# Kernel optimization log

Measured on AMD Instinct MI355X. Metric: run time of the kernel, lower is better.

Reference implementation:

```python
import jax, jax.numpy as jnp
import numpy as np

B = 4; T = 4; C = 1; H = 128; W = 128; P = 16; D = 384; DEPTH = 4
DIN = 768; N = 16; DTR = 24; K = 4
GH = (T * H) // P; GW = W // P; NTOK = GH * GW; POS = NTOK // 2  # middle cls token
SDIM = 16; ADIM = 4


def setup_inputs() -> dict:
    ks = iter(jax.random.split(jax.random.key(0), 48))
    def rn(shape, s=0.02):
        return jax.random.normal(next(ks), shape, jnp.float32) * s
    inp = {}
    inp["depth_seq"] = jax.random.normal(next(ks), (B, T, C, H, W), jnp.float32)
    inp["state_vec"] = jax.random.normal(next(ks), (B, SDIM), jnp.float32)
    inp["action"] = jax.random.normal(next(ks), (B, ADIM), jnp.float32)
    inp["patch_w"] = rn((D, C * P * P)); inp["patch_b"] = jnp.zeros((D,), jnp.float32)
    inp["cls_token"] = rn((1, 1, D)); inp["pos_embed"] = rn((1, NTOK + 1, D))
    inp["ln_w"] = jnp.ones((DEPTH, D), jnp.float32); inp["ln_b"] = jnp.zeros((DEPTH, D), jnp.float32)
    inp["in_proj_w"] = rn((DEPTH, 2 * DIN, D))
    inp["conv_w"] = rn((DEPTH, DIN, K), 0.2); inp["conv_b"] = jnp.zeros((DEPTH, DIN), jnp.float32)
    inp["conv_wb"] = rn((DEPTH, DIN, K), 0.2); inp["conv_bb"] = jnp.zeros((DEPTH, DIN), jnp.float32)
    inp["xproj_w"] = rn((DEPTH, DTR + 2 * N, DIN)); inp["xproj_wb"] = rn((DEPTH, DTR + 2 * N, DIN))
    inp["dtproj_w"] = rn((DEPTH, DIN, DTR), 0.1); inp["dtproj_b"] = jnp.full((DEPTH, DIN), -4.0, jnp.float32)
    inp["dtproj_wb"] = rn((DEPTH, DIN, DTR), 0.1); inp["dtproj_bb"] = jnp.full((DEPTH, DIN), -4.0, jnp.float32)
    Ainit = jnp.log(jnp.tile(jnp.arange(1, N + 1, dtype=jnp.float32)[None, None, :], (DEPTH, DIN, 1)))
    inp["A_log"] = Ainit; inp["A_logb"] = Ainit
    inp["Dp"] = jnp.ones((DEPTH, DIN), jnp.float32); inp["Dpb"] = jnp.ones((DEPTH, DIN), jnp.float32)
    inp["out_w"] = rn((DEPTH, D, DIN))
    inp["lnf_w"] = jnp.ones((D,), jnp.float32); inp["lnf_b"] = jnp.zeros((D,), jnp.float32)
    inp["cw1"] = rn((D, SDIM + ADIM), 0.1); inp["cb1"] = jnp.zeros((D,), jnp.float32)
    inp["cw2"] = rn((D, D), 0.05); inp["cb2"] = jnp.zeros((D,), jnp.float32)
    return inp


def _layernorm(x, w, b):
    m = jnp.mean(x, -1, keepdims=True)
    v = jnp.mean(jnp.square(x - m), -1, keepdims=True)
    return (x - m) * jax.lax.rsqrt(v + 1e-5) * w + b


def _causal_conv(x, w, b):
    # x: [B, L, DIN] depthwise causal conv, kernel K
    L = x.shape[1]
    xp = jnp.pad(x, ((0, 0), (K - 1, 0), (0, 0)))
    y = sum(xp[:, k:k + L, :] * w[:, k] for k in range(K))
    return y + b


def _ssm(xc, dt, Bm, Cm, A, Dv, z):
    # xc, dt, z: [B, L, DIN]; Bm, Cm: [B, L, N]; A, : [DIN, N]; Dv: [DIN]
    dA = jnp.exp(dt[..., None] * A)                                  # [B,L,DIN,N]
    dBx = dt[..., None] * Bm[:, :, None, :] * xc[..., None]          # [B,L,DIN,N]
    def step(h, inp):
        dA_t, dBx_t, C_t = inp
        h = dA_t * h + dBx_t
        return h, jnp.einsum('bdn,bn->bd', h, C_t)
    h0 = jnp.zeros((xc.shape[0], DIN, N), xc.dtype)
    _, ys = jax.lax.scan(step, h0, (jnp.swapaxes(dA, 0, 1), jnp.swapaxes(dBx, 0, 1), jnp.swapaxes(Cm, 0, 1)))
    y = jnp.swapaxes(ys, 0, 1) + xc * Dv
    return y * jax.nn.silu(z)


def _branch(x, z, cw, cb, xw, dw, db, Al, Dv):
    xc = jax.nn.silu(_causal_conv(x, cw, cb))
    xdb = jnp.einsum('bld,ed->ble', xc, xw)
    dt, Bm, Cm = xdb[..., :DTR], xdb[..., DTR:DTR + N], xdb[..., DTR + N:]
    dt = jax.nn.softplus(jnp.einsum('blr,dr->bld', dt, dw) + db)
    return _ssm(xc, dt, Bm, Cm, -jnp.exp(Al), Dv, z)


def _forward(depth_seq, state_vec, action, patch_w, patch_b, cls_token, pos_embed,
             ln_w, ln_b, in_proj_w, conv_w, conv_b, conv_wb, conv_bb,
             xproj_w, xproj_wb, dtproj_w, dtproj_b, dtproj_wb, dtproj_bb,
             A_log, A_logb, Dp, Dpb, out_w, lnf_w, lnf_b, cw1, cb1, cw2, cb2):
    # merge temporal frames vertically: [B,T,C,H,W] -> [B,C,T*H,W]
    img = depth_seq.reshape(B, C, T * H, W)
    # patch embed (conv with kernel=stride=P as a GEMM)
    xr = img.reshape(B, C, GH, P, GW, P).transpose(0, 2, 4, 1, 3, 5).reshape(B, NTOK, C * P * P)
    tok = xr @ patch_w.T + patch_b
    cls = jnp.broadcast_to(cls_token, (B, 1, D))
    tok = jnp.concatenate([tok[:, :POS], cls, tok[:, POS:]], axis=1) + pos_embed
    hidden, residual = tok, None
    for i in range(DEPTH):
        residual = hidden if residual is None else hidden + residual
        h = _layernorm(residual, ln_w[i], ln_b[i])
        xz = jnp.einsum('bld,ed->ble', h, in_proj_w[i])
        x, z = xz[..., :DIN], xz[..., DIN:]
        yf = _branch(x, z, conv_w[i], conv_b[i], xproj_w[i], dtproj_w[i], dtproj_b[i], A_log[i], Dp[i])
        yb = _branch(jnp.flip(x, 1), jnp.flip(z, 1), conv_wb[i], conv_bb[i], xproj_wb[i],
                     dtproj_wb[i], dtproj_bb[i], A_logb[i], Dpb[i])
        hidden = jnp.einsum('ble,de->bld', yf + jnp.flip(yb, 1), out_w[i])
    residual = hidden + residual
    h = _layernorm(residual, lnf_w, lnf_b)
    vis = h[:, POS]
    cmd = jnp.concatenate([state_vec, action], axis=-1)
    cmd = jax.nn.relu(cmd @ cw1.T + cb1) @ cw2.T + cb2
    return vis + cmd


def reference(depth_seq, state_vec, action, patch_w, patch_b, cls_token, pos_embed,
              ln_w, ln_b, in_proj_w, conv_w, conv_b, conv_wb, conv_bb,
              xproj_w, xproj_wb, dtproj_w, dtproj_b, dtproj_wb, dtproj_bb,
              A_log, A_logb, Dp, Dpb, out_w, lnf_w, lnf_b, cw1, cb1, cw2, cb2):
    return _forward(depth_seq, state_vec, action, patch_w, patch_b, cls_token, pos_embed,
                    ln_w, ln_b, in_proj_w, conv_w, conv_b, conv_wb, conv_bb,
                    xproj_w, xproj_wb, dtproj_w, dtproj_b, dtproj_wb, dtproj_bb,
                    A_log, A_logb, Dp, Dpb, out_w, lnf_w, lnf_b, cw1, cb1, cw2, cb2)
```

## Files before the change

kernel.cpp:

```cpp
#include <hip/hip_runtime.h>
#include <hip/hip_bf16.h>
#include <math.h>

#define BB 4
#define LF 257
#define MR 1028
#define DMODEL 384
#define DIN 768
#define NST 16
#define DTR 24
#define XDB 56
#define POSROW 128
#define CL 16
#define NC 17
#define NKC 12

typedef __attribute__((ext_vector_type(8))) short short8;
typedef __attribute__((ext_vector_type(4))) float f32x4;

__device__ __forceinline__ float siluf(float v) { return v / (1.f + __expf(-v)); }
__device__ __forceinline__ float softplusf(float v) {
    return (v > 20.f) ? v : log1pf(__expf(v));
}
__device__ __forceinline__ short f2bf(float f) {
    unsigned u = __builtin_bit_cast(unsigned, f);
    unsigned r = (u + 0x7FFFu + ((u >> 16) & 1u)) >> 16;
    return (short)r;
}

template<int AMODE, int SMODE, int KSTEP, int NBUF>
__device__ __forceinline__ void mgemm_core(
    const float* __restrict__ A, int lda,
    const float* __restrict__ W,
    const float* __restrict__ bias,
    float* __restrict__ Cout, int M, int N, int K, int kb, int ke,
    int bm, int bn,
    const float* __restrict__ gA, const float* __restrict__ A2,
    const float* __restrict__ pos,
    short* __restrict__ Ab, short* __restrict__ Wb)
{
    constexpr int GPT = KSTEP / 32;
    constexpr int NF4 = KSTEP / 16;

    const int tid = threadIdx.x;
    const int m_s = tid >> 2;
    const int q_s = tid & 3;
    const int lane = tid & 63;
    const int wv = tid >> 6;
    const int wm = (wv >> 1) * 32, wn = (wv & 1) * 32;
    const int qq = lane >> 4, lr = lane & 15;

    f32x4 acc[2][2];
    #pragma unroll
    for (int i = 0; i < 2; ++i)
        #pragma unroll
        for (int j = 0; j < 2; ++j)
            acc[i][j] = f32x4{0.f, 0.f, 0.f, 0.f};

    float2 stf = make_float2(0.f, 0.f);
    if (AMODE == 3) {
        int m = bm + m_s;
        if (m < M) stf = ((const float2*)gA)[m];
    }

    float4 pa[NF4], pw[NF4];
    const float4 z4 = make_float4(0.f, 0.f, 0.f, 0.f);

    auto loadA = [&](int k0) {
        int k = k0 + q_s * (KSTEP / 4);
        int m = bm + m_s;
        if (AMODE == 1) {
            int b = m >> 8, t = m & 255;
            int gh = t >> 3, gw = t & 7;
            #pragma unroll
            for (int i = 0; i < NF4; ++i) {
                int ki = k + i * 4;
                int p1 = ki >> 4, p2 = ki & 15;
                pa[i] = *(const float4*)&gA[(size_t)b * 65536 + gh * 2048
                                            + p1 * 128 + gw * 16 + p2];
            }
        } else if (AMODE == 2) {
            if (m < M && k < K) {
                int b = m / LF, l = m - b * LF;
                const float4* s1 = (const float4*)&A[(size_t)m * lda + k];
                const float4* s2 = (const float4*)&A2[(size_t)(b * LF + (LF - 1 - l)) * lda + k];
                #pragma unroll
                for (int i = 0; i < NF4; ++i) {
                    float4 x = s1[i], y = s2[i];
                    pa[i] = make_float4(x.x + y.x, x.y + y.y, x.z + y.z, x.w + y.w);
                }
            } else {
                #pragma unroll
                for (int i = 0; i < NF4; ++i) pa[i] = z4;
            }
        } else {
            if (m < M && k < K) {
                const float4* rr = (const float4*)&A[(size_t)m * lda + k];
                const float4* ww = (const float4*)&A2[k];
                const float4* bb = (const float4*)&pos[k];
                #pragma unroll
                for (int i = 0; i < NF4; ++i) {
                    float4 r = rr[i], w = ww[i], b0 = bb[i];
                    pa[i] = make_float4((r.x - stf.x) * stf.y * w.x + b0.x,
                                        (r.y - stf.x) * stf.y * w.y + b0.y,
                                        (r.z - stf.x) * stf.y * w.z + b0.z,
                                        (r.w - stf.x) * stf.y * w.w + b0.w);
                }
            } else {
                #pragma unroll
                for (int i = 0; i < NF4; ++i) pa[i] = z4;
            }
        }
    };
    auto loadW = [&](int k0) {
        int k = k0 + q_s * (KSTEP / 4);
        int n = bn + m_s;
        if (n < N && k < K) {
            const float4* src = (const float4*)&W[(size_t)n * K + k];
            #pragma unroll
            for (int i = 0; i < NF4; ++i) pw[i] = src[i];
        } else {
            #pragma unroll
            for (int i = 0; i < NF4; ++i) pw[i] = z4;
        }
    };
    auto cvt8 = [&](float4 a, float4 b) -> short8 {
        short8 r;
        r[0] = f2bf(a.x); r[1] = f2bf(a.y); r[2] = f2bf(a.z); r[3] = f2bf(a.w);
        r[4] = f2bf(b.x); r[5] = f2bf(b.y); r[6] = f2bf(b.z); r[7] = f2bf(b.w);
        return r;
    };

    loadA(kb);
    loadW(kb);

    int s = 0;
    for (int k0 = kb; k0 < ke; k0 += KSTEP, ++s) {
        const int buf = (NBUF == 2) ? (s & 1) * (KSTEP * 64) : 0;
        #pragma unroll
        for (int g = 0; g < GPT; ++g) {
            *(short8*)&Ab[buf + ((q_s * GPT + g) * 64 + m_s) * 8] = cvt8(pa[2 * g], pa[2 * g + 1]);
            *(short8*)&Wb[buf + ((q_s * GPT + g) * 64 + m_s) * 8] = cvt8(pw[2 * g], pw[2 * g + 1]);
        }
        __syncthreads();
        if (k0 + KSTEP < ke) { loadA(k0 + KSTEP); loadW(k0 + KSTEP); }
        #pragma unroll
        for (int kh = 0; kh < GPT; ++kh) {
            const int kg = kh * 4 + qq;
            short8 af0 = *(const short8*)&Ab[buf + (kg * 64 + wm + lr) * 8];
            short8 af1 = *(const short8*)&Ab[buf + (kg * 64 + wm + 16 + lr) * 8];
            short8 wf0 = *(const short8*)&Wb[buf + (kg * 64 + wn + lr) * 8];
            short8 wf1 = *(const short8*)&Wb[buf + (kg * 64 + wn + 16 + lr) * 8];
            acc[0][0] = __builtin_amdgcn_mfma_f32_16x16x32_bf16(af0, wf0, acc[0][0], 0, 0, 0);
            acc[0][1] = __builtin_amdgcn_mfma_f32_16x16x32_bf16(af0, wf1, acc[0][1], 0, 0, 0);
            acc[1][0] = __builtin_amdgcn_mfma_f32_16x16x32_bf16(af1, wf0, acc[1][0], 0, 0, 0);
            acc[1][1] = __builtin_amdgcn_mfma_f32_16x16x32_bf16(af1, wf1, acc[1][1], 0, 0, 0);
        }
        if (NBUF == 1 && k0 + KSTEP < ke) __syncthreads();
    }

    #pragma unroll
    for (int mi = 0; mi < 2; ++mi) {
        #pragma unroll
        for (int ni = 0; ni < 2; ++ni) {
            int col = bn + wn + ni * 16 + lr;
            if (col >= N) continue;
            #pragma unroll
            for (int r = 0; r < 4; ++r) {
                int row = bm + wm + mi * 16 + qq * 4 + r;
                if (row >= M) continue;
                float v = acc[mi][ni][r];
                if (SMODE == 0) {
                    if (bias) v += bias[col];
                    Cout[(size_t)row * N + col] = v;
                } else if (SMODE == 3) {
                    int b = row >> 8, t = row & 255;
                    int l = (t < POSROW) ? t : t + 1;
                    v += bias[col] + pos[(size_t)l * DMODEL + col];
                    Cout[(size_t)(b * LF + l) * DMODEL + col] = v;
                } else {
                    atomicAdd(&Cout[(size_t)row * N + col], v);
                }
            }
        }
    }
}

template<int AMODE, int SMODE, int KSTEP, int NBUF>
__global__ __launch_bounds__(256) void mgemm_k(
    const float* __restrict__ A, int lda,
    const float* __restrict__ W, const float* __restrict__ bias,
    float* __restrict__ Cout, int M, int N, int K, int KS,
    const float* __restrict__ gA, const float* __restrict__ A2,
    const float* __restrict__ pos,
    float* __restrict__ zbuf, int zcount)
{
    __shared__ __align__(16) short Ab[NBUF * KSTEP * 64];
    __shared__ __align__(16) short Wb[NBUF * KSTEP * 64];
    if (zbuf) {
        int nthr = gridDim.x * gridDim.y * 256;
        int gi = (blockIdx.x + blockIdx.y * gridDim.x) * 256 + threadIdx.x;
        for (int i = gi; i < zcount; i += nthr) zbuf[i] = 0.f;
    }
    int nwg = gridDim.x * gridDim.y;
    int lin = blockIdx.x + blockIdx.y * gridDim.x;
    if ((nwg & 7) == 0) {
        int ch = nwg >> 3;
        lin = (lin & 7) * ch + (lin >> 3);
    }
    int bx = lin % gridDim.x;
    int by = lin / gridDim.x;
    int ntile = by / KS, ks = by % KS;
    int chunk = K / KS;
    mgemm_core<AMODE, SMODE, KSTEP, NBUF>(A, lda, W, bias, Cout, M, N, K,
                             ks * chunk, ks * chunk + chunk, bx * 64, ntile * 64,
                             gA, A2, pos, Ab, Wb);
}

__global__ __launch_bounds__(256) void xp_k(
    const float* __restrict__ xz,
    const float* __restrict__ cwf, const float* __restrict__ cbf,
    const float* __restrict__ cwb, const float* __restrict__ cbb,
    const float* __restrict__ Wf, const float* __restrict__ Wb,
    float* __restrict__ xcf, float* __restrict__ xcb,
    float* __restrict__ xdbf, float* __restrict__ xdbb)
{
    __shared__ __align__(16) short Ash[4096];
    __shared__ __align__(16) short Wsh[4096];
    const int br = blockIdx.z;
    const int kcid = blockIdx.y;
    const float* cw = br ? cwb : cwf;
    const float* cbv = br ? cbb : cbf;
    const float* W  = br ? Wb  : Wf;
    float* xco      = br ? xcb : xcf;
    float* xdo      = br ? xdbb : xdbf;

    const int tid = threadIdx.x;
    const int m_s = tid >> 2, q_s = tid & 3;
    const int bm = blockIdx.x * 64;
    const int kb = kcid * 64;
    const int lane = tid & 63, wv = tid >> 6;
    const int wm = (wv >> 1) * 32, wn = (wv & 1) * 32;
    const int qq = lane >> 4, lr = lane & 15;
    const int m = bm + m_s;
    const bool mok = (m < MR);
    int b = 0, l = 0;
    if (mok) { b = m / LF; l = m - b * LF; }

    const int d0 = kb + q_s * 16;
    float a16[16];
    if (mok) {
        #pragma unroll
        for (int i = 0; i < 4; ++i) {
            float4 c = ((const float4*)&cbv[d0])[i];
            a16[4 * i] = c.x; a16[4 * i + 1] = c.y;
            a16[4 * i + 2] = c.z; a16[4 * i + 3] = c.w;
        }
        float wreg[16][4];
        #pragma unroll
        for (int j = 0; j < 16; ++j)
            *(float4*)wreg[j] = *(const float4*)&cw[(d0 + j) * 4];
        #pragma unroll
        for (int kk = 0; kk < 4; ++kk) {
            int li = l - 3 + kk;
            if (li >= 0) {
                int srow = br ? (b * LF + (LF - 1 - li)) : (b * LF + li);
                const float4* xp = (const float4*)&xz[(size_t)srow * 2 * DIN + d0];
                #pragma unroll
                for (int i = 0; i < 4; ++i) {
                    float4 x = xp[i];
                    a16[4 * i]     += x.x * wreg[4 * i][kk];
                    a16[4 * i + 1] += x.y * wreg[4 * i + 1][kk];
                    a16[4 * i + 2] += x.z * wreg[4 * i + 2][kk];
                    a16[4 * i + 3] += x.w * wreg[4 * i + 3][kk];
                }
            }
        }
        #pragma unroll
        for (int j = 0; j < 16; ++j) a16[j] = siluf(a16[j]);
    } else {
        #pragma unroll
        for (int j = 0; j < 16; ++j) a16[j] = 0.f;
    }

    float4 pw[4];
    {
        const float4 z4 = make_float4(0.f, 0.f, 0.f, 0.f);
        if (m_s < XDB) {
            const float4* src = (const float4*)&W[(size_t)m_s * DIN + kb + q_s * 16];
            pw[0] = src[0]; pw[1] = src[1]; pw[2] = src[2]; pw[3] = src[3];
        } else { pw[0] = z4; pw[1] = z4; pw[2] = z4; pw[3] = z4; }
    }

    auto cvt8a = [&](int o) -> short8 {
        short8 r;
        #pragma unroll
        for (int j = 0; j < 8; ++j) r[j] = f2bf(a16[o + j]);
        return r;
    };
    auto cvt8w = [&](float4 a, float4 b) -> short8 {
        short8 r;
        r[0] = f2bf(a.x); r[1] = f2bf(a.y); r[2] = f2bf(a.z); r[3] = f2bf(a.w);
        r[4] = f2bf(b.x); r[5] = f2bf(b.y); r[6] = f2bf(b.z); r[7] = f2bf(b.w);
        return r;
    };

    *(short8*)&Ash[((2 * q_s) * 64 + m_s) * 8]     = cvt8a(0);
    *(short8*)&Ash[((2 * q_s + 1) * 64 + m_s) * 8] = cvt8a(8);
    *(short8*)&Wsh[((2 * q_s) * 64 + m_s) * 8]     = cvt8w(pw[0], pw[1]);
    *(short8*)&Wsh[((2 * q_s + 1) * 64 + m_s) * 8] = cvt8w(pw[2], pw[3]);
    if (mok) {
        float4* dst = (float4*)&xco[(size_t)m * DIN + d0];
        dst[0] = make_float4(a16[0], a16[1], a16[2], a16[3]);
        dst[1] = make_float4(a16[4], a16[5], a16[6], a16[7]);
        dst[2] = make_float4(a16[8], a16[9], a16[10], a16[11]);
        dst[3] = make_float4(a16[12], a16[13], a16[14], a16[15]);
    }
    __syncthreads();

    f32x4 acc[2][2];
    #pragma unroll
    for (int i = 0; i < 2; ++i)
        #pragma unroll
        for (int j = 0; j < 2; ++j)
            acc[i][j] = f32x4{0.f, 0.f, 0.f, 0.f};

    #pragma unroll
    for (int kh = 0; kh < 2; ++kh) {
        const int kg = kh * 4 + qq;
        short8 af0 = *(const short8*)&Ash[(kg * 64 + wm + lr) * 8];
        short8 af1 = *(const short8*)&Ash[(kg * 64 + wm + 16 + lr) * 8];
        short8 wf0 = *(const short8*)&Wsh[(kg * 64 + wn + lr) * 8];
        short8 wf1 = *(const short8*)&Wsh[(kg * 64 + wn + 16 + lr) * 8];
        acc[0][0] = __builtin_amdgcn_mfma_f32_16x16x32_bf16(af0, wf0, acc[0][0], 0, 0, 0);
        acc[0][1] = __builtin_amdgcn_mfma_f32_16x16x32_bf16(af0, wf1, acc[0][1], 0, 0, 0);
        acc[1][0] = __builtin_amdgcn_mfma_f32_16x16x32_bf16(af1, wf0, acc[1][0], 0, 0, 0);
        acc[1][1] = __builtin_amdgcn_mfma_f32_16x16x32_bf16(af1, wf1, acc[1][1], 0, 0, 0);
    }

    #pragma unroll
    for (int mi = 0; mi < 2; ++mi) {
        #pragma unroll
        for (int ni = 0; ni < 2; ++ni) {
            int col = wn + ni * 16 + lr;
            if (col >= XDB) continue;
            #pragma unroll
            for (int r = 0; r < 4; ++r) {
                int row = bm + wm + mi * 16 + qq * 4 + r;
                if (row >= MR) continue;
                atomicAdd(&xdo[(size_t)row * XDB + col], acc[mi][ni][r]);
            }
        }
    }
}

__global__ void cls_k(const float* __restrict__ cls, const float* __restrict__ pos,
                      float* __restrict__ residual) {
    int b = blockIdx.x, t = threadIdx.x;
    residual[(size_t)(b * LF + POSROW) * DMODEL + t] =
        cls[t] + pos[(size_t)POSROW * DMODEL + t];
}

__global__ __launch_bounds__(128) void lnstat_k(const float* __restrict__ X,
                                                float2* __restrict__ st) {
    int r = blockIdx.x;
    const float* x = X + (size_t)r * DMODEL;
    int t = threadIdx.x;
    float v0 = x[t], v1 = x[t + 128], v2 = x[t + 256];
    float s = v0 + v1 + v2;
    float sq = v0 * v0 + v1 * v1 + v2 * v2;
    #pragma unroll
    for (int o = 32; o > 0; o >>= 1) {
        s += __shfl_down(s, o);
        sq += __shfl_down(sq, o);
    }
    __shared__ float ls[2], lq[2];
    if ((t & 63) == 0) { ls[t >> 6] = s; lq[t >> 6] = sq; }
    __syncthreads();
    if (t == 0) {
        float S = ls[0] + ls[1], Q = lq[0] + lq[1];
        float mean = S * (1.f / 384.f);
        float var = Q * (1.f / 384.f) - mean * mean;
        st[r] = make_float2(mean, rsqrtf(var + 1e-5f));
    }
}

__global__ __launch_bounds__(256) void scanA_k(
    const float* __restrict__ xcf, const float* __restrict__ xcb,
    const float* __restrict__ xdbf, const float* __restrict__ xdbb,
    const float* __restrict__ alf, const float* __restrict__ alb,
    const float* __restrict__ dwf, const float* __restrict__ dbf,
    const float* __restrict__ dwb, const float* __restrict__ dbb,
    float* __restrict__ hpart, float* __restrict__ sumd) {
    const int t = threadIdx.x;
    const int half = t & 1, dl = t >> 1;
    const int y = blockIdx.y;
    const int b = y >> 1, br = y & 1;
    const int c = blockIdx.z;
    const int d = blockIdx.x * 128 + dl;
    const float* xc  = br ? xcb  : xcf;
    const float* xdb = br ? xdbb : xdbf;
    const float* Al  = br ? alb  : alf;
    const float* dw  = br ? dwb  : dwf;
    const float* dbi = br ? dbb  : dbf;

    float An[8];
    #pragma unroll
    for (int n = 0; n < 8; ++n)
        An[n] = -__expf(Al[(size_t)d * NST + half * 8 + n]);
    float wdt[DTR];
    #pragma unroll
    for (int k = 0; k < DTR; k += 4)
        *(float4*)&wdt[k] = *(const float4*)&dw[(size_t)d * DTR + k];
    float dbv = dbi[d];

    float xr[CL];
    #pragma unroll
    for (int s = 0; s < CL; ++s) {
        int l = c * CL + s;
        xr[s] = (l < LF) ? xc[(size_t)(b * LF + l) * DIN + d] : 0.f;
    }

    __shared__ float sXD[CL][DTR];
    __shared__ float sB[CL][NST];
    for (int idx = t; idx < CL * DTR; idx += 256) {
        int s0 = idx / DTR, j0 = idx - s0 * DTR;
        int l0 = c * CL + s0;
        sXD[s0][j0] = (l0 < LF) ? xdb[(size_t)(b * LF + l0) * XDB + j0] : 0.f;
    }
    {
        int s0 = t >> 4, j0 = t & 15;
        int l0 = c * CL + s0;
        sB[s0][j0] = (l0 < LF) ? xdb[(size_t)(b * LF + l0) * XDB + DTR + j0] : 0.f;
    }
    __syncthreads();

    float h[8] = {};
    float sdt = 0.f;
    #pragma unroll
    for (int s = 0; s < CL; ++s) {
        int l = c * CL + s;
        if (l < LF) {
            float dtv = dbv;
            #pragma unroll
            for (int k = 0; k < DTR; ++k) dtv += sXD[s][k] * wdt[k];
            dtv = softplusf(dtv);
            sdt += dtv;
            float dtx = dtv * xr[s];
            #pragma unroll
            for (int n = 0; n < 8; ++n)
                h[n] = __expf(dtv * An[n]) * h[n] + dtx * sB[s][half * 8 + n];
        }
    }
    size_t base = (size_t)(c * 8 + y) * NST;
    #pragma unroll
    for (int n = 0; n < 8; ++n)
        hpart[(base + half * 8 + n) * DIN + d] = h[n];
    if (half == 0) sumd[(size_t)(c * 8 + y) * DIN + d] = sdt;
}

__global__ __launch_bounds__(256) void scanC_k(
    const float* __restrict__ xcf, const float* __restrict__ xcb,
    const float* __restrict__ xdbf, const float* __restrict__ xdbb,
    const float* __restrict__ xz,
    const float* __restrict__ alf, const float* __restrict__ dpf,
    const float* __restrict__ alb, const float* __restrict__ dpb,
    const float* __restrict__ dwf, const float* __restrict__ dbf,
    const float* __restrict__ dwb, const float* __restrict__ dbb,
    const float* __restrict__ hpart, const float* __restrict__ sumd,
    float* __restrict__ yf, float* __restrict__ yb) {
    const int t = threadIdx.x;
    const int half = t & 1, dl = t >> 1;
    const int y = blockIdx.y;
    const int b = y >> 1, br = y & 1;
    const int c = blockIdx.z;
    const int d = blockIdx.x * 128 + dl;
    const float* xc  = br ? xcb  : xcf;
    const float* xdb = br ? xdbb : xdbf;
    const float* Al  = br ? alb  : alf;
    const float* Dpp = br ? dpb  : dpf;
    const float* dw  = br ? dwb  : dwf;
    const float* dbi = br ? dbb  : dbf;
    float* yo        = br ? yb   : yf;

    float An[8];
    #pragma unroll
    for (int n = 0; n < 8; ++n)
        An[n] = -__expf(Al[(size_t)d * NST + half * 8 + n]);
    float wdt[DTR];
    #pragma unroll
    for (int k = 0; k < DTR; k += 4)
        *(float4*)&wdt[k] = *(const float4*)&dw[(size_t)d * DTR + k];
    float dbv = dbi[d];
    float Dv = Dpp[d];

    float xr[CL], zr[CL];
    #pragma unroll
    for (int s = 0; s < CL; ++s) {
        int l = c * CL + s;
        if (l < LF) {
            xr[s] = xc[(size_t)(b * LF + l) * DIN + d];
            int zl = br ? (LF - 1 - l) : l;
            zr[s] = xz[(size_t)(b * LF + zl) * (2 * DIN) + DIN + d];
        } else { xr[s] = 0.f; zr[s] = 0.f; }
    }

    __shared__ float sXD[CL][DTR];
    __shared__ float sB[CL][NST];
    __shared__ float sC[CL][NST];
    for (int idx = t; idx < CL * DTR; idx += 256) {
        int s0 = idx / DTR, j0 = idx - s0 * DTR;
        int l0 = c * CL + s0;
        sXD[s0][j0] = (l0 < LF) ? xdb[(size_t)(b * LF + l0) * XDB + j0] : 0.f;
    }
    {
        int s0 = t >> 4, j0 = t & 15;
        int l0 = c * CL + s0;
        size_t rb = (size_t)(b * LF + l0) * XDB + DTR;
        sB[s0][j0] = (l0 < LF) ? xdb[rb + j0] : 0.f;
        sC[s0][j0] = (l0 < LF) ? xdb[rb + NST + j0] : 0.f;
    }
    __syncthreads();

    float h[8] = {};
    for (int j = 0; j < c; ++j) {
        float sd = sumd[(size_t)(j * 8 + y) * DIN + d];
        size_t bj = (size_t)(j * 8 + y) * NST;
        #pragma unroll
        for (int n = 0; n < 8; ++n)
            h[n] = __expf(An[n] * sd) * h[n] + hpart[(bj + half * 8 + n) * DIN + d];
    }

    #pragma unroll
    for (int s = 0; s < CL; ++s) {
        int l = c * CL + s;
        if (l < LF) {
            int row = b * LF + l;
            float dtv = dbv;
            #pragma unroll
            for (int k = 0; k < DTR; ++k) dtv += sXD[s][k] * wdt[k];
            dtv = softplusf(dtv);
            float dtx = dtv * xr[s];
            float acc = 0.f;
            #pragma unroll
            for (int n = 0; n < 8; ++n) {
                h[n] = __expf(dtv * An[n]) * h[n] + dtx * sB[s][half * 8 + n];
                acc += h[n] * sC[s][half * 8 + n];
            }
            acc += __shfl_xor(acc, 1);
            if (half == 0)
                yo[(size_t)row * DIN + d] = (acc + xr[s] * Dv) * siluf(zr[s]);
        }
    }
}

__global__ __launch_bounds__(384) void final_k(
    const float* __restrict__ residual,
    const float* __restrict__ lnw, const float* __restrict__ lnb,
    const float* __restrict__ sv, const float* __restrict__ act,
    const float* __restrict__ cw1, const float* __restrict__ cb1,
    const float* __restrict__ cw2, const float* __restrict__ cb2,
    float* __restrict__ out) {
    int b = blockIdx.x, t = threadIdx.x;
    const float* x = residual + (size_t)(b * LF + POSROW) * DMODEL;
    float v = x[t];
    float s = v, sq = v * v;
    #pragma unroll
    for (int o = 32; o > 0; o >>= 1) {
        s += __shfl_down(s, o);
        sq += __shfl_down(sq, o);
    }
    __shared__ float ls[6], lq[6], hid[DMODEL], cmdin[20];
    if ((t & 63) == 0) { ls[t >> 6] = s; lq[t >> 6] = sq; }
    if (t < 20) cmdin[t] = (t < 16) ? sv[b * 16 + t] : act[b * 4 + t - 16];
    __syncthreads();
    float S = 0.f, Q = 0.f;
    #pragma unroll
    for (int w = 0; w < 6; ++w) { S += ls[w]; Q += lq[w]; }
    float mean = S * (1.f / 384.f);
    float var = Q * (1.f / 384.f) - mean * mean;
    float rs = rsqrtf(var + 1e-5f);
    float vis = (v - mean) * rs * lnw[t] + lnb[t];
    float a1 = cb1[t];
    #pragma unroll
    for (int k = 0; k < 20; ++k) a1 += cmdin[k] * cw1[t * 20 + k];
    hid[t] = fmaxf(a1, 0.f);
    __syncthreads();
    float a2 = cb2[t];
    for (int k = 0; k < DMODEL; ++k) a2 += hid[k] * cw2[t * DMODEL + k];
    out[b * DMODEL + t] = vis + a2;
}

extern "C" void kernel_launch(void* const* d_in, const int* in_sizes, int n_in,
                              void* d_out, int out_size, void* d_ws, size_t ws_size,
                              hipStream_t stream) {
    const float* depth_seq = (const float*)d_in[0];
    const float* state_vec = (const float*)d_in[1];
    const float* action    = (const float*)d_in[2];
    const float* patch_w   = (const float*)d_in[3];
    const float* patch_b   = (const float*)d_in[4];
    const float* cls_token = (const float*)d_in[5];
    const float* pos_embed = (const float*)d_in[6];
    const float* ln_w      = (const float*)d_in[7];
    const float* ln_b      = (const float*)d_in[8];
    const float* in_proj_w = (const float*)d_in[9];
    const float* conv_w    = (const float*)d_in[10];
    const float* conv_b    = (const float*)d_in[11];
    const float* conv_wb   = (const float*)d_in[12];
    const float* conv_bb   = (const float*)d_in[13];
    const float* xproj_w   = (const float*)d_in[14];
    const float* xproj_wb  = (const float*)d_in[15];
    const float* dtproj_w  = (const float*)d_in[16];
    const float* dtproj_b  = (const float*)d_in[17];
    const float* dtproj_wb = (const float*)d_in[18];
    const float* dtproj_bb = (const float*)d_in[19];
    const float* A_log     = (const float*)d_in[20];
    const float* A_logb    = (const float*)d_in[21];
    const float* Dp        = (const float*)d_in[22];
    const float* Dpb       = (const float*)d_in[23];
    const float* out_w     = (const float*)d_in[24];
    const float* lnf_w     = (const float*)d_in[25];
    const float* lnf_b     = (const float*)d_in[26];
    const float* cw1       = (const float*)d_in[27];
    const float* cb1       = (const float*)d_in[28];
    const float* cw2       = (const float*)d_in[29];
    const float* cb2       = (const float*)d_in[30];

    float* ws = (float*)d_ws;
    size_t o = 0;
    float* residual = ws + o; o += (size_t)MR * DMODEL;
    float* xz       = ws + o; o += (size_t)MR * 2 * DIN;
    float* xcf      = ws + o; o += (size_t)MR * DIN;
    float* xcb      = ws + o; o += (size_t)MR * DIN;
    float* xdbf     = ws + o; o += (size_t)MR * XDB;
    float* xdbb     = ws + o; o += (size_t)MR * XDB;
    float* yfb      = ws + o; o += (size_t)MR * DIN;
    float* ybb      = ws + o; o += (size_t)MR * DIN;
    float* hpart    = ws + o; o += (size_t)NC * 8 * NST * DIN;
    float* sumd     = ws + o; o += (size_t)NC * 8 * DIN;
    float2* stats   = (float2*)(ws + o); o += (size_t)MR * 2;
    (void)ws_size; (void)in_sizes; (void)n_in; (void)out_size;

    mgemm_k<1, 3, 128, 2><<<dim3(16, 6), 256, 0, stream>>>(
        nullptr, 0, patch_w, patch_b, residual, 1024, DMODEL, 256, 1,
        depth_seq, nullptr, pos_embed, nullptr, 0);
    cls_k<<<BB, DMODEL, 0, stream>>>(cls_token, pos_embed, residual);

    for (int i = 0; i < 4; ++i) {
        lnstat_k<<<MR, 128, 0, stream>>>(residual, stats);
        mgemm_k<3, 0, 128, 2><<<dim3(17, 24), 256, 0, stream>>>(
            residual, DMODEL, in_proj_w + (size_t)i * 2 * DIN * DMODEL, nullptr,
            xz, MR, 2 * DIN, DMODEL, 1,
            (const float*)stats, ln_w + (size_t)i * DMODEL, ln_b + (size_t)i * DMODEL,
            xdbf, 2 * MR * XDB);
        xp_k<<<dim3(17, NKC, 2), 256, 0, stream>>>(
            xz, conv_w + (size_t)i * DIN * 4, conv_b + (size_t)i * DIN,
            conv_wb + (size_t)i * DIN * 4, conv_bb + (size_t)i * DIN,
            xproj_w + (size_t)i * XDB * DIN, xproj_wb + (size_t)i * XDB * DIN,
            xcf, xcb, xdbf, xdbb);
        scanA_k<<<dim3(6, 8, NC), 256, 0, stream>>>(
            xcf, xcb, xdbf, xdbb,
            A_log + (size_t)i * DIN * NST, A_logb + (size_t)i * DIN * NST,
            dtproj_w + (size_t)i * DIN * DTR, dtproj_b + (size_t)i * DIN,
            dtproj_wb + (size_t)i * DIN * DTR, dtproj_bb + (size_t)i * DIN,
            hpart, sumd);
        scanC_k<<<dim3(6, 8, NC), 256, 0, stream>>>(
            xcf, xcb, xdbf, xdbb, xz,
            A_log + (size_t)i * DIN * NST, Dp + (size_t)i * DIN,
            A_logb + (size_t)i * DIN * NST, Dpb + (size_t)i * DIN,
            dtproj_w + (size_t)i * DIN * DTR, dtproj_b + (size_t)i * DIN,
            dtproj_wb + (size_t)i * DIN * DTR, dtproj_bb + (size_t)i * DIN,
            hpart, sumd, yfb, ybb);
        mgemm_k<2, 4, 192, 1><<<dim3(17, 6 * 4), 256, 0, stream>>>(
            yfb, DIN, out_w + (size_t)i * DMODEL * DIN, nullptr,
            residual, MR, DMODEL, DIN, 4, nullptr, ybb, nullptr, nullptr, 0);
    }

    final_k<<<BB, DMODEL, 0, stream>>>(
        residual, lnf_w, lnf_b, state_vec, action, cw1, cb1, cw2, cb2,
        (float*)d_out);
}
```

Before: 590.6 us.

## Cache softplus dt from scanA, restructure chunk carry combine, retune GEMM templates

scanA now writes the softplus-activated dt values to two new workspace buffers, and scanC reads them back, so it no longer recomputes the 24-wide dt projection or loads the dt slice into shared memory. The carry-in loop in scanC now walks the earlier chunks in reverse, accumulating a suffix sum of decay so each chunk's partial state contributes independently rather than through a serial multiply chain. The mgemm template parameters also change for the patch, in_proj and out_proj GEMMs (for example 128 to 64, and 192,1 to 64,2). Storing and reloading dt adds roughly 2×MR×DIN floats of extra global traffic per layer in exchange for the removed arithmetic.

```diff
diff --git a/kernel.cpp b/kernel.cpp
--- a/kernel.cpp
+++ b/kernel.cpp
@@ -391,7 +391,8 @@
     const float* __restrict__ alf, const float* __restrict__ alb,
     const float* __restrict__ dwf, const float* __restrict__ dbf,
     const float* __restrict__ dwb, const float* __restrict__ dbb,
-    float* __restrict__ hpart, float* __restrict__ sumd) {
+    float* __restrict__ hpart, float* __restrict__ sumd,
+    float* __restrict__ dtf, float* __restrict__ dtb) {
     const int t = threadIdx.x;
     const int half = t & 1, dl = t >> 1;
     const int y = blockIdx.y;
@@ -403,6 +404,7 @@
     const float* Al  = br ? alb  : alf;
     const float* dw  = br ? dwb  : dwf;
     const float* dbi = br ? dbb  : dbf;
+    float* dto       = br ? dtb  : dtf;
 
     float An[8];
     #pragma unroll
@@ -445,6 +447,7 @@
             #pragma unroll
             for (int k = 0; k < DTR; ++k) dtv += sXD[s][k] * wdt[k];
             dtv = softplusf(dtv);
+            if (half == 0) dto[(size_t)(b * LF + l) * DIN + d] = dtv;
             sdt += dtv;
             float dtx = dtv * xr[s];
             #pragma unroll
@@ -465,8 +468,7 @@
     const float* __restrict__ xz,
     const float* __restrict__ alf, const float* __restrict__ dpf,
     const float* __restrict__ alb, const float* __restrict__ dpb,
-    const float* __restrict__ dwf, const float* __restrict__ dbf,
-    const float* __restrict__ dwb, const float* __restrict__ dbb,
+    const float* __restrict__ dtf, const float* __restrict__ dtb,
     const float* __restrict__ hpart, const float* __restrict__ sumd,
     float* __restrict__ yf, float* __restrict__ yb) {
     const int t = threadIdx.x;
@@ -479,40 +481,30 @@
     const float* xdb = br ? xdbb : xdbf;
     const float* Al  = br ? alb  : alf;
     const float* Dpp = br ? dpb  : dpf;
-    const float* dw  = br ? dwb  : dwf;
-    const float* dbi = br ? dbb  : dbf;
+    const float* dti = br ? dtb  : dtf;
     float* yo        = br ? yb   : yf;
 
     float An[8];
     #pragma unroll
     for (int n = 0; n < 8; ++n)
         An[n] = -__expf(Al[(size_t)d * NST + half * 8 + n]);
-    float wdt[DTR];
-    #pragma unroll
-    for (int k = 0; k < DTR; k += 4)
-        *(float4*)&wdt[k] = *(const float4*)&dw[(size_t)d * DTR + k];
-    float dbv = dbi[d];
     float Dv = Dpp[d];
 
-    float xr[CL], zr[CL];
+    float dtr[CL], xr[CL], zr[CL];
     #pragma unroll
     for (int s = 0; s < CL; ++s) {
         int l = c * CL + s;
         if (l < LF) {
-            xr[s] = xc[(size_t)(b * LF + l) * DIN + d];
+            size_t rowoff = (size_t)(b * LF + l) * DIN + d;
+            dtr[s] = dti[rowoff];
+            xr[s] = xc[rowoff];
             int zl = br ? (LF - 1 - l) : l;
             zr[s] = xz[(size_t)(b * LF + zl) * (2 * DIN) + DIN + d];
-        } else { xr[s] = 0.f; zr[s] = 0.f; }
-    }
-
-    __shared__ float sXD[CL][DTR];
+        } else { dtr[s] = 0.f; xr[s] = 0.f; zr[s] = 0.f; }
+    }
+
     __shared__ float sB[CL][NST];
     __shared__ float sC[CL][NST];
-    for (int idx = t; idx < CL * DTR; idx += 256) {
-        int s0 = idx / DTR, j0 = idx - s0 * DTR;
-        int l0 = c * CL + s0;
-        sXD[s0][j0] = (l0 < LF) ? xdb[(size_t)(b * LF + l0) * XDB + j0] : 0.f;
-    }
     {
         int s0 = t >> 4, j0 = t & 15;
         int l0 = c * CL + s0;
@@ -523,12 +515,14 @@
     __syncthreads();
 
     float h[8] = {};
-    for (int j = 0; j < c; ++j) {
+    float suf = 0.f;
+    for (int j = c - 1; j >= 0; --j) {
         float sd = sumd[(size_t)(j * 8 + y) * DIN + d];
         size_t bj = (size_t)(j * 8 + y) * NST;
         #pragma unroll
         for (int n = 0; n < 8; ++n)
-            h[n] = __expf(An[n] * sd) * h[n] + hpart[(bj + half * 8 + n) * DIN + d];
+            h[n] += __expf(An[n] * suf) * hpart[(bj + half * 8 + n) * DIN + d];
+        suf += sd;
     }
 
     #pragma unroll
@@ -536,10 +530,7 @@
         int l = c * CL + s;
         if (l < LF) {
             int row = b * LF + l;
-            float dtv = dbv;
-            #pragma unroll
-            for (int k = 0; k < DTR; ++k) dtv += sXD[s][k] * wdt[k];
-            dtv = softplusf(dtv);
+            float dtv = dtr[s];
             float dtx = dtv * xr[s];
             float acc = 0.f;
             #pragma unroll
@@ -638,17 +629,19 @@
     float* ybb      = ws + o; o += (size_t)MR * DIN;
     float* hpart    = ws + o; o += (size_t)NC * 8 * NST * DIN;
     float* sumd     = ws + o; o += (size_t)NC * 8 * DIN;
+    float* dtf      = ws + o; o += (size_t)MR * DIN;
+    float* dtb      = ws + o; o += (size_t)MR * DIN;
     float2* stats   = (float2*)(ws + o); o += (size_t)MR * 2;
     (void)ws_size; (void)in_sizes; (void)n_in; (void)out_size;
 
-    mgemm_k<1, 3, 128, 2><<<dim3(16, 6), 256, 0, stream>>>(
+    mgemm_k<1, 3, 64, 2><<<dim3(16, 6), 256, 0, stream>>>(
         nullptr, 0, patch_w, patch_b, residual, 1024, DMODEL, 256, 1,
         depth_seq, nullptr, pos_embed, nullptr, 0);
     cls_k<<<BB, DMODEL, 0, stream>>>(cls_token, pos_embed, residual);
 
     for (int i = 0; i < 4; ++i) {
         lnstat_k<<<MR, 128, 0, stream>>>(residual, stats);
-        mgemm_k<3, 0, 128, 2><<<dim3(17, 24), 256, 0, stream>>>(
+        mgemm_k<3, 0, 64, 2><<<dim3(17, 24), 256, 0, stream>>>(
             residual, DMODEL, in_proj_w + (size_t)i * 2 * DIN * DMODEL, nullptr,
             xz, MR, 2 * DIN, DMODEL, 1,
             (const float*)stats, ln_w + (size_t)i * DMODEL, ln_b + (size_t)i * DMODEL,
@@ -663,15 +656,13 @@
             A_log + (size_t)i * DIN * NST, A_logb + (size_t)i * DIN * NST,
             dtproj_w + (size_t)i * DIN * DTR, dtproj_b + (size_t)i * DIN,
             dtproj_wb + (size_t)i * DIN * DTR, dtproj_bb + (size_t)i * DIN,
-            hpart, sumd);
+            hpart, sumd, dtf, dtb);
         scanC_k<<<dim3(6, 8, NC), 256, 0, stream>>>(
             xcf, xcb, xdbf, xdbb, xz,
             A_log + (size_t)i * DIN * NST, Dp + (size_t)i * DIN,
             A_logb + (size_t)i * DIN * NST, Dpb + (size_t)i * DIN,
-            dtproj_w + (size_t)i * DIN * DTR, dtproj_b + (size_t)i * DIN,
-            dtproj_wb + (size_t)i * DIN * DTR, dtproj_bb + (size_t)i * DIN,
-            hpart, sumd, yfb, ybb);
-        mgemm_k<2, 4, 192, 1><<<dim3(17, 6 * 4), 256, 0, stream>>>(
+            dtf, dtb, hpart, sumd, yfb, ybb);
+        mgemm_k<2, 4, 64, 2><<<dim3(17, 6 * 4), 256, 0, stream>>>(
             yfb, DIN, out_w + (size_t)i * DMODEL * DIN, nullptr,
             residual, MR, DMODEL, DIN, 4, nullptr, ybb, nullptr, nullptr, 0);
     }
```

Measured after the change: 496.7 us, median of 3. 1.19x faster.
